# Kernel tuning notes

Measured on AMD Instinct MI355X. Metric: run time of the kernel, lower is better.

Reference implementation:

```python
import jax, jax.numpy as jnp
import numpy as np

B, T, D, H = 256, 512, 512, 512


def setup_inputs() -> dict:
    key = jax.random.key(0)
    k1, k2, k3, k4 = jax.random.split(key, 4)
    inputs = jax.random.normal(k1, (B, T, D), dtype=jnp.float32)
    lengths = jax.random.randint(k2, (B,), 0, T).astype(jnp.int32)
    # LSTM params. Flax nn.LSTMCell uses per-gate dense layers:
    #  input dense (with bias) and recurrent dense (no bias). Packing the
    #  four gates (i, f, g, o) into one matrix is mathematically identical.
    Wx = jax.random.normal(k3, (D, 4 * H), dtype=jnp.float32) * (1.0 / np.sqrt(D))
    Wh = jax.random.normal(k4, (H, 4 * H), dtype=jnp.float32) * (1.0 / np.sqrt(H))
    b = jnp.zeros((4 * H,), dtype=jnp.float32)
    return {"inputs": inputs, "lengths": lengths, "Wx": Wx, "Wh": Wh, "b": b}


def reference(inputs, lengths, Wx, Wh, b):
    batch = inputs.shape[0]
    hidden = Wh.shape[0]
    x_tbd = jnp.swapaxes(inputs, 0, 1)  # [T, B, D]

    def step(carry, x_t):
        c, h = carry
        # fused gate pre-activations: [B, 4H]
        z = x_t @ Wx + h @ Wh + b
        i, f, g, o = jnp.split(z, 4, axis=-1)
        i = jax.nn.sigmoid(i)
        f = jax.nn.sigmoid(f)
        g = jnp.tanh(g)
        o = jax.nn.sigmoid(o)
        c_new = f * c + i * g
        h_new = o * jnp.tanh(c_new)
        return (c_new, h_new), h_new

    c0 = jnp.zeros((batch, hidden), dtype=inputs.dtype)
    h0 = jnp.zeros((batch, hidden), dtype=inputs.dtype)
    _, hs = jax.lax.scan(step, (c0, h0), x_tbd)  # hs: [T, B, H]

    # select output at last valid timestep per example
    idx = jnp.maximum(0, lengths - 1)  # [B]
    return hs[idx, jnp.arange(batch), :]  # [B, H]
```

## Files before the change

kernel.cpp:

```cpp
#include <hip/hip_runtime.h>

#define Bb 256
#define Tt 512
#define Dd 512
#define Hh 512
#define KTOT 1024
#define FOURH 2048

typedef __attribute__((ext_vector_type(8))) short bf16x8;
typedef __attribute__((ext_vector_type(4))) float f32x4;

__device__ __forceinline__ unsigned short f2bf(float f) {
    union { float f; unsigned u; } x; x.f = f;
    unsigned u = x.u;
    unsigned r = u + 0x7FFFu + ((u >> 16) & 1u);
    return (unsigned short)(r >> 16);
}
__device__ __forceinline__ float bf2f(unsigned short s) {
    union { unsigned u; float f; } x; x.u = ((unsigned)s) << 16;
    return x.f;
}

__device__ __forceinline__ uint4 load16_sc01(const void* p) {
    uint4 v;
    asm volatile("global_load_dwordx4 %0, %1, off sc0 sc1" : "=v"(v) : "v"(p));
    return v;
}

__device__ __forceinline__ void i16_to_bf(int v, unsigned short& bh, unsigned short& bl) {
    int vh = v >> 8;
    int vl = v & 255;
    union { float f; unsigned u; } a, b;
    a.f = (float)vh * 0.0078125f;
    b.f = (float)vl * 3.0517578125e-05f;
    bh = (unsigned short)(a.u >> 16);
    bl = (unsigned short)(b.u >> 16);
}

__global__ void prep_w(const float* __restrict__ Wx, const float* __restrict__ Wh,
                       unsigned short* __restrict__ WT_hi, unsigned short* __restrict__ WT_lo) {
    __shared__ float tile[32][33];
    int n0 = (blockIdx.x & 63) * 32;
    int k0 = (blockIdx.x >> 6) * 32;
    int tx = threadIdx.x & 31;
    int ty = threadIdx.x >> 5;
    for (int q = 0; q < 4; ++q) {
        int k = k0 + ty + q * 8;
        int n = n0 + tx;
        float v = (k < Dd) ? Wx[(size_t)k * FOURH + n] : Wh[(size_t)(k - Dd) * FOURH + n];
        tile[ty + q * 8][tx] = v;
    }
    __syncthreads();
    for (int q = 0; q < 4; ++q) {
        int nl = ty + q * 8;
        int kl = tx;
        float v = tile[kl][nl];
        unsigned short hi = f2bf(v);
        unsigned short lo = f2bf(v - bf2f(hi));
        size_t o = (size_t)(n0 + nl) * KTOT + (size_t)(k0 + kl);
        WT_hi[o] = hi;
        WT_lo[o] = lo;
    }
}

__global__ void init_state3(char* __restrict__ ws, int persist) {
    long i = (long)blockIdx.x * blockDim.x + threadIdx.x;
    if (i < 98304) {
        *(uint4*)(ws + (8u << 20) + i * 16) = (uint4){0, 0, 0, 0};
    }
    if (persist && i < 512) {
        ((unsigned int*)(ws + (8u << 20) + (1536u << 10)))[i] = 0u;
    }
}

__global__ __launch_bounds__(512) void lstm_persist11(
    const float* __restrict__ X, const int* __restrict__ lengths,
    const unsigned short* __restrict__ WT_hi, const unsigned short* __restrict__ WT_lo,
    const float* __restrict__ bias,
    short* __restrict__ h_i16,
    unsigned int* __restrict__ ctrl,
    float* __restrict__ out)
{
    __shared__ unsigned short HLDS[32768];
    __shared__ unsigned short XLDS[32768];
    __shared__ float zbuf[8][32][17];

    const int bx = blockIdx.x;
    const int group = bx & 7;
    const int slot = bx >> 3;
    const int rt = slot & 7;
    const int cs = slot >> 3;
    const int r0 = rt * 32;
    const int j0h = group * 64 + cs * 16;
    const int tid = threadIdx.x;
    const int w8 = tid >> 6;
    const int lane = tid & 63;
    const int l15 = lane & 15;
    const int q4 = lane >> 4;
    const int klo = q4 * 8;
    const int gate = w8 & 3;
    const int khalf = w8 >> 2;

    const size_t HB = (size_t)Bb * Hh;

    const int colg = gate * 512 + j0h + l15;
    const size_t bbase = (size_t)colg * KTOT + (size_t)khalf * 512;
    const unsigned short* bhp = &WT_hi[bbase];
    const unsigned short* blp = &WT_lo[bbase];

    const int xr = tid >> 4;
    const int xk0 = (tid & 15) * 32;
    const float* xbase = &X[((size_t)(r0 + xr) * Tt) * Dd + xk0];

    const int er = tid >> 4;
    const int ej = tid & 15;
    const int row_g = r0 + er;
    const int col_h = j0h + ej;
    const size_t oidx = (size_t)row_g * Hh + col_h;
    int oT = lengths[row_g] - 1; if (oT < 0) oT = 0;
    const float b0 = bias[col_h], b1 = bias[512 + col_h],
                b2 = bias[1024 + col_h], b3 = bias[1536 + col_h];
    float creg = 0.f;

    unsigned int* myflag = &ctrl[rt * 32];

    for (int t = 0; t < Tt; ++t) {
        const int p_r = t & 1;
        const short* hp_r = h_i16 + (size_t)p_r * HB;
        short* hp_w = h_i16 + (size_t)(p_r ^ 1) * HB;

        uint4 hb[4];
#pragma unroll
        for (int it = 0; it < 4; ++it) {
            const int c = it * 512 + tid;
            const int row = c >> 6, k8 = c & 63;
            hb[it] = load16_sc01(hp_r + (size_t)(r0 + row) * Hh + k8 * 8);
        }

        {
            const float* xp = xbase + (size_t)t * Dd;
            float4 xv[8];
#pragma unroll
            for (int i = 0; i < 8; ++i) xv[i] = ((const float4*)xp)[i];
            const int ksx = tid & 15;
            const int mi = xr >> 4, lr = xr & 15;
#pragma unroll
            for (int c2 = 0; c2 < 4; ++c2) {
                float vv[8];
                *(float4*)&vv[0] = xv[2 * c2];
                *(float4*)&vv[4] = xv[2 * c2 + 1];
                bf16x8 hv8, lv8;
#pragma unroll
                for (int e = 0; e < 8; ++e) {
                    unsigned short hs = f2bf(vv[e]);
                    hv8[e] = (short)hs;
                    lv8[e] = (short)f2bf(vv[e] - bf2f(hs));
                }
                const int lnw = (c2 * 16 + lr) ^ (ksx & 7);
                *(bf16x8*)&XLDS[(((0 * 2 + mi) * 16 + ksx) * 64 + lnw) * 8] = hv8;
                *(bf16x8*)&XLDS[(((1 * 2 + mi) * 16 + ksx) * 64 + lnw) * 8] = lv8;
            }
        }

        asm volatile("s_waitcnt vmcnt(0)" ::: "memory");
        __builtin_amdgcn_sched_barrier(0);

#pragma unroll
        for (int it = 0; it < 4; ++it) {
            const int c = it * 512 + tid;
            const int row = c >> 6, k8 = c & 63;
            const int ksh = k8 >> 2, qq = k8 & 3;
            const int mi = row >> 4, lr = row & 15;
            const uint4 q = hb[it];
            const unsigned qs[4] = {q.x, q.y, q.z, q.w};
            bf16x8 ahv, alv;
#pragma unroll
            for (int e = 0; e < 4; ++e) {
                const unsigned u = qs[e];
                unsigned short bh0, bl0, bh1, bl1;
                i16_to_bf((int)(short)(u & 0xffffu), bh0, bl0);
                i16_to_bf((int)(short)(u >> 16), bh1, bl1);
                ahv[2 * e] = (short)bh0; alv[2 * e] = (short)bl0;
                ahv[2 * e + 1] = (short)bh1; alv[2 * e + 1] = (short)bl1;
            }
            const int lnw = (qq * 16 + lr) ^ (ksh & 7);
            *(bf16x8*)&HLDS[(((0 * 2 + mi) * 16 + ksh) * 64 + lnw) * 8] = ahv;
            *(bf16x8*)&HLDS[(((1 * 2 + mi) * 16 + ksh) * 64 + lnw) * 8] = alv;
        }
        __syncthreads();

        const unsigned short* ALDS = khalf ? HLDS : XLDS;
        f32x4 acc[2][3];
#pragma unroll
        for (int mi = 0; mi < 2; ++mi)
#pragma unroll
            for (int s = 0; s < 3; ++s)
                acc[mi][s] = (f32x4){0.f, 0.f, 0.f, 0.f};

#pragma unroll
        for (int ks = 0; ks < 16; ++ks) {
            const int kk = ks * 32 + klo;
            const bf16x8 bh = *(const bf16x8*)&bhp[kk];
            const bf16x8 bl = *(const bf16x8*)&blp[kk];
            const int lnr = lane ^ (ks & 7);
#pragma unroll
            for (int mi = 0; mi < 2; ++mi) {
                const bf16x8 ah = *(const bf16x8*)&ALDS[(((0 * 2 + mi) * 16 + ks) * 64 + lnr) * 8];
                const bf16x8 al = *(const bf16x8*)&ALDS[(((1 * 2 + mi) * 16 + ks) * 64 + lnr) * 8];
                acc[mi][0] = __builtin_amdgcn_mfma_f32_16x16x32_bf16(ah, bh, acc[mi][0], 0, 0, 0);
                acc[mi][1] = __builtin_amdgcn_mfma_f32_16x16x32_bf16(ah, bl, acc[mi][1], 0, 0, 0);
                acc[mi][2] = __builtin_amdgcn_mfma_f32_16x16x32_bf16(al, bh, acc[mi][2], 0, 0, 0);
            }
        }

#pragma unroll
        for (int mi = 0; mi < 2; ++mi) {
            const f32x4 z = acc[mi][0] + acc[mi][1] + acc[mi][2];
#pragma unroll
            for (int r = 0; r < 4; ++r)
                zbuf[w8][mi * 16 + q4 * 4 + r][l15] = z[r];
        }
        __syncthreads();

        float zi = zbuf[0][er][ej] + zbuf[4][er][ej] + b0;
        float zf = zbuf[1][er][ej] + zbuf[5][er][ej] + b1;
        float zg = zbuf[2][er][ej] + zbuf[6][er][ej] + b2;
        float zo = zbuf[3][er][ej] + zbuf[7][er][ej] + b3;
        float ig = 1.f / (1.f + expf(-zi));
        float fg = 1.f / (1.f + expf(-zf));
        float gg = tanhf(zg);
        float og = 1.f / (1.f + expf(-zo));
        float cn = fg * creg + ig * gg;
        creg = cn;
        float hn = og * tanhf(cn);
        int vi = __float2int_rn(hn * 32768.f);
        vi = vi > 32767 ? 32767 : (vi < -32767 ? -32767 : vi);
        __hip_atomic_store(&hp_w[oidx], (short)vi, __ATOMIC_RELAXED, __HIP_MEMORY_SCOPE_SYSTEM);
        if (t == oT) out[oidx] = hn;

        if (t < Tt - 1) {
            asm volatile("s_waitcnt vmcnt(0)" ::: "memory");
            __syncthreads();
            if (tid == 0) {
                __hip_atomic_fetch_add(myflag, 1u, __ATOMIC_RELAXED, __HIP_MEMORY_SCOPE_SYSTEM);
                const unsigned int tgt = (unsigned int)(t + 1) * 32u;
                while (__hip_atomic_load(myflag, __ATOMIC_RELAXED, __HIP_MEMORY_SCOPE_SYSTEM) < tgt)
                    __builtin_amdgcn_s_sleep(2);
            }
            __syncthreads();
        }
    }
}

__global__ __launch_bounds__(512) void lstm_step4(
    const float* __restrict__ X, const int* __restrict__ lengths,
    const unsigned short* __restrict__ WT_hi, const unsigned short* __restrict__ WT_lo,
    const float* __restrict__ bias,
    float* __restrict__ c_st,
    const unsigned short* __restrict__ h_r_hi, const unsigned short* __restrict__ h_r_lo,
    unsigned short* __restrict__ h_w_hi, unsigned short* __restrict__ h_w_lo,
    float* __restrict__ out, int t)
{
    __shared__ float zbuf[8][16][17];

    const int bx = blockIdx.x;
    const int xcd = bx & 7;
    const int rem = bx >> 3;
    const int m0 = (rem & 15) * 16;
    const int col_group = xcd * 4 + (rem >> 4);
    const int hc0 = col_group * 16;
    const int tid = threadIdx.x;
    const int w8 = tid >> 6;
    const int lane = tid & 63;
    const int gate = w8 & 3;
    const int khalf = w8 >> 2;

    f32x4 ahh = (f32x4){0,0,0,0}, ahl = (f32x4){0,0,0,0}, alh = (f32x4){0,0,0,0};

    const int colk = gate * 512 + hc0 + (lane & 15);
    const size_t bbase = (size_t)colk * KTOT;
    const int klo = (lane >> 4) * 8;
    const int row = m0 + (lane & 15);

    if (khalf == 0) {
        const float* xrow = &X[((size_t)row * Tt + t) * Dd];
        const unsigned short* bhp = &WT_hi[bbase];
        const unsigned short* blp = &WT_lo[bbase];
#pragma unroll
        for (int ks = 0; ks < 16; ++ks) {
            const int kk = ks * 32 + klo;
            const float4 v0 = *(const float4*)&xrow[kk];
            const float4 v1 = *(const float4*)&xrow[kk + 4];
            float vv[8] = {v0.x, v0.y, v0.z, v0.w, v1.x, v1.y, v1.z, v1.w};
            bf16x8 ah, al;
#pragma unroll
            for (int e = 0; e < 8; ++e) {
                unsigned short hi = f2bf(vv[e]);
                ah[e] = (short)hi;
                al[e] = (short)f2bf(vv[e] - bf2f(hi));
            }
            const bf16x8 bh = *(const bf16x8*)&bhp[kk];
            const bf16x8 bl = *(const bf16x8*)&blp[kk];
            ahh = __builtin_amdgcn_mfma_f32_16x16x32_bf16(ah, bh, ahh, 0, 0, 0);
            ahl = __builtin_amdgcn_mfma_f32_16x16x32_bf16(ah, bl, ahl, 0, 0, 0);
            alh = __builtin_amdgcn_mfma_f32_16x16x32_bf16(al, bh, alh, 0, 0, 0);
        }
    } else {
        const unsigned short* hrh = &h_r_hi[(size_t)row * Hh];
        const unsigned short* hrl = &h_r_lo[(size_t)row * Hh];
        const unsigned short* bhp = &WT_hi[bbase + 512];
        const unsigned short* blp = &WT_lo[bbase + 512];
#pragma unroll
        for (int ks = 0; ks < 16; ++ks) {
            const int kk = ks * 32 + klo;
            const bf16x8 ah = *(const bf16x8*)&hrh[kk];
            const bf16x8 al = *(const bf16x8*)&hrl[kk];
            const bf16x8 bh = *(const bf16x8*)&bhp[kk];
            const bf16x8 bl = *(const bf16x8*)&blp[kk];
            ahh = __builtin_amdgcn_mfma_f32_16x16x32_bf16(ah, bh, ahh, 0, 0, 0);
            ahl = __builtin_amdgcn_mfma_f32_16x16x32_bf16(ah, bl, ahl, 0, 0, 0);
            alh = __builtin_amdgcn_mfma_f32_16x16x32_bf16(al, bh, alh, 0, 0, 0);
        }
    }

    const f32x4 z = ahh + ahl + alh;
#pragma unroll
    for (int r = 0; r < 4; ++r)
        zbuf[w8][(lane >> 4) * 4 + r][lane & 15] = z[r];
    __syncthreads();

    if (tid < 256) {
        const int r = tid >> 4;
        const int j = tid & 15;
        const int row_g = m0 + r;
        const int col_g = hc0 + j;
        float zi = zbuf[0][r][j] + zbuf[4][r][j] + bias[col_g];
        float zf = zbuf[1][r][j] + zbuf[5][r][j] + bias[512 + col_g];
        float zg = zbuf[2][r][j] + zbuf[6][r][j] + bias[1024 + col_g];
        float zo = zbuf[3][r][j] + zbuf[7][r][j] + bias[1536 + col_g];
        float ig = 1.f / (1.f + expf(-zi));
        float fg = 1.f / (1.f + expf(-zf));
        float gg = tanhf(zg);
        float og = 1.f / (1.f + expf(-zo));
        const size_t idx = (size_t)row_g * Hh + col_g;
        float cn = fg * c_st[idx] + ig * gg;
        float hn = og * tanhf(cn);
        c_st[idx] = cn;
        unsigned short hh = f2bf(hn);
        h_w_hi[idx] = hh;
        h_w_lo[idx] = f2bf(hn - bf2f(hh));
        int len = lengths[row_g];
        int oidx = len - 1; if (oidx < 0) oidx = 0;
        if (t == oidx) out[idx] = hn;
    }
}

extern "C" void kernel_launch(void* const* d_in, const int* in_sizes, int n_in,
                              void* d_out, int out_size, void* d_ws, size_t ws_size,
                              hipStream_t stream) {
    const float* X = (const float*)d_in[0];
    const int* lengths = (const int*)d_in[1];
    const float* Wx = (const float*)d_in[2];
    const float* Wh = (const float*)d_in[3];
    const float* bias = (const float*)d_in[4];
    float* out = (float*)d_out;

    char* ws = (char*)d_ws;
    unsigned short* WT_hi = (unsigned short*)ws;
    unsigned short* WT_lo = (unsigned short*)(ws + (4u << 20));
    short* h_i16 = (short*)(ws + (8u << 20));
    unsigned int* ctrl = (unsigned int*)(ws + (8u << 20) + (1536u << 10));
    float* c_st = (float*)(ws + (8u << 20));
    unsigned short* h_base = (unsigned short*)(ws + (8u << 20) + (512u << 10));
    const size_t HB = (size_t)Bb * Hh;
    unsigned short* h_hi0 = h_base;
    unsigned short* h_lo0 = h_base + HB;
    unsigned short* h_hi1 = h_base + 2 * HB;
    unsigned short* h_lo1 = h_base + 3 * HB;

    const size_t NEED_PERSIST = (8u << 20) + (1536u << 10) + 4096u;
    const int can_persist = (ws_size >= NEED_PERSIST) ? 1 : 0;

    hipLaunchKernelGGL(prep_w, dim3(2048), dim3(256), 0, stream, Wx, Wh, WT_hi, WT_lo);
    hipLaunchKernelGGL(init_state3, dim3(512), dim3(256), 0, stream, ws, can_persist);

    hipError_t err = hipErrorUnknown;
    if (can_persist) {
        void* args[] = { (void*)&X, (void*)&lengths, (void*)&WT_hi, (void*)&WT_lo,
                         (void*)&bias, (void*)&h_i16, (void*)&ctrl, (void*)&out };
        err = hipLaunchCooperativeKernel((const void*)lstm_persist11,
                                         dim3(256), dim3(512), args, 0, stream);
    }
    if (err != hipSuccess) {
        for (int t = 0; t < Tt; ++t) {
            const bool even = (t & 1) == 0;
            hipLaunchKernelGGL(lstm_step4, dim3(512), dim3(512), 0, stream,
                               X, lengths, WT_hi, WT_lo, bias, c_st,
                               even ? h_hi0 : h_hi1, even ? h_lo0 : h_lo1,
                               even ? h_hi1 : h_hi0, even ? h_lo1 : h_lo0,
                               out, t);
        }
    }
}
```

Measured before the change: 6.529 ms.

## Replace shared atomic counter barrier with per-block flags and overlap X staging

```diff
diff --git a/kernel.cpp b/kernel.cpp
--- a/kernel.cpp
+++ b/kernel.cpp
@@ -68,12 +68,12 @@
     if (i < 98304) {
         *(uint4*)(ws + (8u << 20) + i * 16) = (uint4){0, 0, 0, 0};
     }
-    if (persist && i < 512) {
+    if (persist && i < 4096) {
         ((unsigned int*)(ws + (8u << 20) + (1536u << 10)))[i] = 0u;
     }
 }
 
-__global__ __launch_bounds__(512) void lstm_persist11(
+__global__ __launch_bounds__(512) void lstm_persist12(
     const float* __restrict__ X, const int* __restrict__ lengths,
     const unsigned short* __restrict__ WT_hi, const unsigned short* __restrict__ WT_lo,
     const float* __restrict__ bias,
@@ -111,6 +111,8 @@
     const int xr = tid >> 4;
     const int xk0 = (tid & 15) * 32;
     const float* xbase = &X[((size_t)(r0 + xr) * Tt) * Dd + xk0];
+    const int ksx = tid & 15;
+    const int xmi = xr >> 4, xlr = xr & 15;
 
     const int er = tid >> 4;
     const int ej = tid & 15;
@@ -122,7 +124,33 @@
                 b2 = bias[1024 + col_h], b3 = bias[1536 + col_h];
     float creg = 0.f;
 
-    unsigned int* myflag = &ctrl[rt * 32];
+    const int wgIdx = group * 4 + cs;
+    unsigned int* myflag = ctrl + ((size_t)(rt * 32 + wgIdx)) * 16;
+    const unsigned int* flagbase = ctrl + (size_t)rt * 32 * 16;
+    const unsigned int* pollp = flagbase + (size_t)(lane & 31) * 16;
+
+    {
+        const float* xp = xbase;
+        float4 xv[8];
+#pragma unroll
+        for (int i = 0; i < 8; ++i) xv[i] = ((const float4*)xp)[i];
+#pragma unroll
+        for (int c2 = 0; c2 < 4; ++c2) {
+            float vv[8];
+            *(float4*)&vv[0] = xv[2 * c2];
+            *(float4*)&vv[4] = xv[2 * c2 + 1];
+            bf16x8 hv8, lv8;
+#pragma unroll
+            for (int e = 0; e < 8; ++e) {
+                unsigned short hs = f2bf(vv[e]);
+                hv8[e] = (short)hs;
+                lv8[e] = (short)f2bf(vv[e] - bf2f(hs));
+            }
+            const int lnw = (c2 * 16 + xlr) ^ (ksx & 7);
+            *(bf16x8*)&XLDS[(((0 * 2 + xmi) * 16 + ksx) * 64 + lnw) * 8] = hv8;
+            *(bf16x8*)&XLDS[(((1 * 2 + xmi) * 16 + ksx) * 64 + lnw) * 8] = lv8;
+        }
+    }
 
     for (int t = 0; t < Tt; ++t) {
         const int p_r = t & 1;
@@ -135,31 +163,6 @@
             const int c = it * 512 + tid;
             const int row = c >> 6, k8 = c & 63;
             hb[it] = load16_sc01(hp_r + (size_t)(r0 + row) * Hh + k8 * 8);
-        }
-
-        {
-            const float* xp = xbase + (size_t)t * Dd;
-            float4 xv[8];
-#pragma unroll
-            for (int i = 0; i < 8; ++i) xv[i] = ((const float4*)xp)[i];
-            const int ksx = tid & 15;
-            const int mi = xr >> 4, lr = xr & 15;
-#pragma unroll
-            for (int c2 = 0; c2 < 4; ++c2) {
-                float vv[8];
-                *(float4*)&vv[0] = xv[2 * c2];
-                *(float4*)&vv[4] = xv[2 * c2 + 1];
-                bf16x8 hv8, lv8;
-#pragma unroll
-                for (int e = 0; e < 8; ++e) {
-                    unsigned short hs = f2bf(vv[e]);
-                    hv8[e] = (short)hs;
-                    lv8[e] = (short)f2bf(vv[e] - bf2f(hs));
-                }
-                const int lnw = (c2 * 16 + lr) ^ (ksx & 7);
-                *(bf16x8*)&XLDS[(((0 * 2 + mi) * 16 + ksx) * 64 + lnw) * 8] = hv8;
-                *(bf16x8*)&XLDS[(((1 * 2 + mi) * 16 + ksx) * 64 + lnw) * 8] = lv8;
-            }
         }
 
         asm volatile("s_waitcnt vmcnt(0)" ::: "memory");
@@ -241,11 +244,40 @@
         if (t < Tt - 1) {
             asm volatile("s_waitcnt vmcnt(0)" ::: "memory");
             __syncthreads();
-            if (tid == 0) {
-                __hip_atomic_fetch_add(myflag, 1u, __ATOMIC_RELAXED, __HIP_MEMORY_SCOPE_SYSTEM);
-                const unsigned int tgt = (unsigned int)(t + 1) * 32u;
-                while (__hip_atomic_load(myflag, __ATOMIC_RELAXED, __HIP_MEMORY_SCOPE_SYSTEM) < tgt)
+            if (tid == 0)
+                __hip_atomic_store(myflag, (unsigned)(t + 1), __ATOMIC_RELAXED,
+                                   __HIP_MEMORY_SCOPE_SYSTEM);
+
+            {
+                const float* xp = xbase + (size_t)(t + 1) * Dd;
+                float4 xv[8];
+#pragma unroll
+                for (int i = 0; i < 8; ++i) xv[i] = ((const float4*)xp)[i];
+#pragma unroll
+                for (int c2 = 0; c2 < 4; ++c2) {
+                    float vv[8];
+                    *(float4*)&vv[0] = xv[2 * c2];
+                    *(float4*)&vv[4] = xv[2 * c2 + 1];
+                    bf16x8 hv8, lv8;
+#pragma unroll
+                    for (int e = 0; e < 8; ++e) {
+                        unsigned short hs = f2bf(vv[e]);
+                        hv8[e] = (short)hs;
+                        lv8[e] = (short)f2bf(vv[e] - bf2f(hs));
+                    }
+                    const int lnw = (c2 * 16 + xlr) ^ (ksx & 7);
+                    *(bf16x8*)&XLDS[(((0 * 2 + xmi) * 16 + ksx) * 64 + lnw) * 8] = hv8;
+                    *(bf16x8*)&XLDS[(((1 * 2 + xmi) * 16 + ksx) * 64 + lnw) * 8] = lv8;
+                }
+            }
+
+            if (w8 == 0) {
+                while (true) {
+                    unsigned v = __hip_atomic_load(pollp, __ATOMIC_RELAXED,
+                                                   __HIP_MEMORY_SCOPE_SYSTEM);
+                    if (__all(v >= (unsigned)(t + 1))) break;
                     __builtin_amdgcn_s_sleep(2);
+                }
             }
             __syncthreads();
         }
@@ -378,7 +410,7 @@
     unsigned short* h_hi1 = h_base + 2 * HB;
     unsigned short* h_lo1 = h_base + 3 * HB;
 
-    const size_t NEED_PERSIST = (8u << 20) + (1536u << 10) + 4096u;
+    const size_t NEED_PERSIST = (8u << 20) + (1536u << 10) + 32768u;
     const int can_persist = (ws_size >= NEED_PERSIST) ? 1 : 0;
 
     hipLaunchKernelGGL(prep_w, dim3(2048), dim3(256), 0, stream, Wx, Wh, WT_hi, WT_lo);
@@ -388,7 +420,7 @@
     if (can_persist) {
         void* args[] = { (void*)&X, (void*)&lengths, (void*)&WT_hi, (void*)&WT_lo,
                          (void*)&bias, (void*)&h_i16, (void*)&ctrl, (void*)&out };
-        err = hipLaunchCooperativeKernel((const void*)lstm_persist11,
+        err = hipLaunchCooperativeKernel((const void*)lstm_persist12,
                                          dim3(256), dim3(512), args, 0, stream);
     }
     if (err != hipSuccess) {
```

Result: faster. 6.112 ms, median of 2 (-6.4%).
